# Kernel tuning notes

Hardware: AMD Instinct MI355X
Metric: run time of the kernel (lower is better)

Reference implementation:

```python
import jax, jax.numpy as jnp
import numpy as np

VOCAB = 512
EMB = 256
HID = 64
T_HORIZON = 0.05


def setup_inputs() -> dict:
    key = jax.random.key(0)
    ks = jax.random.split(key, 6)
    B, L = 32, 4096
    x = jax.random.randint(ks[0], (B, L), 0, VOCAB, dtype=jnp.int64 if jax.config.jax_enable_x64 else jnp.int32)
    emb_table = jax.random.normal(ks[1], (VOCAB, EMB), dtype=jnp.float32)
    W1 = jax.random.normal(ks[2], (EMB, HID), dtype=jnp.float32) * (1.0 / np.sqrt(EMB))
    b1 = jnp.zeros((HID,), dtype=jnp.float32)
    W2 = jax.random.normal(ks[3], (HID, VOCAB), dtype=jnp.float32) * (1.0 / np.sqrt(HID))
    b2 = jnp.full((VOCAB,), 0.1, dtype=jnp.float32)  # torch: bias.data.fill_(0.1)
    return {"x": x, "emb_table": emb_table, "W1": W1, "b1": b1, "W2": W2, "b2": b2, "steps": 5}


def reference(x, emb_table, W1, b1, W2, b2, steps):
    """Vectorized Gillespie-style Markov jump simulation.

    Equivalent to the torch loop: intensity is computed once per step from the
    current state, then every (b, l) position samples a candidate next state
    from softmax(intensity) with the self-transition zeroed and renormalized
    (== categorical over logits with the current state masked to -inf), and
    accepts it with prob 1 - exp(-rate * dt).
    """
    V = emb_table.shape[0]
    dt = T_HORIZON / steps
    key = jax.random.key(42)
    keys = jax.random.split(key, steps)
    vocab_ids = jnp.arange(V)

    def step(x_t, k):
        # intensity: [B, L, V]
        h = jax.nn.relu(emb_table[x_t] @ W1 + b1)
        intensity = h @ W2 + b2
        # mask self-transition (softmax * (1 - onehot) then renormalize)
        self_mask = x_t[..., None] == vocab_ids  # [B, L, V] bool
        masked_logits = jnp.where(self_mask, -jnp.inf, intensity)
        k1, k2 = jax.random.split(k)
        next_state = jax.random.categorical(k1, masked_logits)  # [B, L]
        rate = jnp.take_along_axis(intensity, next_state[..., None], axis=-1)[..., 0]
        accept_prob = 1.0 - jnp.exp(-rate * dt)
        u = jax.random.uniform(k2, x_t.shape, dtype=rate.dtype)
        x_t = jnp.where(u < accept_prob, next_state.astype(x_t.dtype), x_t)
        return x_t, None

    x_final, _ = jax.lax.scan(step, x, keys)
    return x_final
```

## Files before the change

### kernel.cpp

```cpp
#include <hip/hip_runtime.h>
#include <stdint.h>


#define VOCAB  512
#define EMB    256
#define HID    64
#define NPOS   (32 * 4096)
#define STEPS  5
#define PPW    8
#define CHUNKS (NPOS / PPW)
#define MBLK   2048
#define CPB    (CHUNKS / MBLK)

__host__ __device__ __forceinline__ void tf2x32(uint32_t k0, uint32_t k1,
                                                uint32_t x0, uint32_t x1,
                                                uint32_t& o0, uint32_t& o1) {
  uint32_t ks2 = k0 ^ k1 ^ 0x1BD11BDAu;
  x0 += k0; x1 += k1;
#define TFR(r) { x0 += x1; x1 = (x1 << (r)) | (x1 >> (32 - (r))); x1 ^= x0; }
  TFR(13) TFR(15) TFR(26) TFR(6)
  x0 += k1;  x1 += ks2 + 1u;
  TFR(17) TFR(29) TFR(16) TFR(24)
  x0 += ks2; x1 += k0 + 2u;
  TFR(13) TFR(15) TFR(26) TFR(6)
  x0 += k0;  x1 += k1 + 3u;
  TFR(17) TFR(29) TFR(16) TFR(24)
  x0 += k1;  x1 += ks2 + 4u;
  TFR(13) TFR(15) TFR(26) TFR(6)
  x0 += ks2; x1 += k0 + 5u;
#undef TFR
  o0 = x0; o1 = x1;
}

struct Keys {
  uint32_t k1a[STEPS], k1b[STEPS];
  uint32_t k2a[STEPS], k2b[STEPS];
};

__global__ __launch_bounds__(512)
void build_table(const float* __restrict__ emb,
                 const float* __restrict__ W1,
                 const float* __restrict__ b1,
                 const float* __restrict__ W2,
                 const float* __restrict__ b2,
                 float* __restrict__ I,
                 float* __restrict__ pthr) {
  const int s   = blockIdx.x;
  const int tid = threadIdx.x;
  __shared__ double part[8][HID];
  __shared__ double hd[HID];
  __shared__ float  redmax[8];

  const int hid = tid & (HID - 1);
  const int kq  = tid >> 6;
  const float* e = emb + s * EMB;
  double acc = 0.0;
#pragma unroll
  for (int ib = 0; ib < 32; ib += 16) {
    float ev[16], wv[16];
#pragma unroll
    for (int i = 0; i < 16; ++i) {
      const int k = kq + 8 * (ib + i);
      ev[i] = e[k];
      wv[i] = W1[k * HID + hid];
    }
#pragma unroll
    for (int i = 0; i < 16; ++i)
      acc += (double)ev[i] * (double)wv[i];
  }
  part[kq][hid] = acc;
  __syncthreads();
  if (kq == 0) {
    const double a = ((part[0][hid] + part[1][hid]) + (part[2][hid] + part[3][hid]))
                   + ((part[4][hid] + part[5][hid]) + (part[6][hid] + part[7][hid]));
    const float m = (float)a + b1[hid];
    hd[hid] = (double)(m > 0.0f ? m : 0.0f);
  }
  __syncthreads();

  double acc2 = 0.0;
#pragma unroll
  for (int kb = 0; kb < HID; kb += 16) {
    float wv[16];
#pragma unroll
    for (int i = 0; i < 16; ++i)
      wv[i] = W2[(kb + i) * VOCAB + tid];
#pragma unroll
    for (int i = 0; i < 16; ++i)
      acc2 += hd[kb + i] * (double)wv[i];
  }
  const float val = (float)acc2 + b2[tid];
  I[s * VOCAB + tid] = val;

  float lmax = val;
  for (int off = 32; off > 0; off >>= 1)
    lmax = fmaxf(lmax, __shfl_xor(lmax, off, 64));
  if ((tid & 63) == 0) redmax[tid >> 6] = lmax;
  __syncthreads();
  if (tid == 0) {
    float m = redmax[0];
#pragma unroll
    for (int i = 1; i < 8; ++i) m = fmaxf(m, redmax[i]);
    const float z = (-m) * 0.01f;
    pthr[s] = 1.0f - (float)exp((double)z);
  }
}

__global__ __launch_bounds__(256)
void markov_kernel(const int* __restrict__ x_in,
                   const float* __restrict__ I,
                   const float* __restrict__ pthr,
                   int* __restrict__ x_out,
                   Keys K) {
  __shared__ int next_chunk;
  if (threadIdx.x == 0) next_chunk = 0;
  __syncthreads();

  const int lane = threadIdx.x & 63;
  const int qp = lane / 5;
  const int qt = lane - qp * 5;
  const float TINYF = 1.17549435e-38f;

  for (;;) {
    int c = 0;
    if (lane == 0) c = atomicAdd(&next_chunk, 1);
    c = __shfl(c, 0, 64);
    if (c >= CPB) break;
    const int base = (blockIdx.x * CPB + c) * PPW;

    int scur = (lane < PPW) ? x_in[base + lane] : 0;
    const float pv = (lane < PPW) ? pthr[scur] : 0.0f;

    float u40 = 0.0f;
    if (lane < PPW * STEPS) {
      uint32_t w0, w1;
      tf2x32(K.k2a[qt], K.k2b[qt], 0u, (uint32_t)(base + qp), w0, w1);
      u40 = __uint_as_float((((w0 ^ w1) >> 9) | 0x3f800000u)) - 1.0f;
    }

    const float pq = __shfl(pv, qp, 64);
    const bool cand = (lane < PPW * STEPS) && (u40 < pq);
    unsigned long long mask = __ballot(cand);

    while (mask) {
      const int q = (int)__builtin_ctzll(mask);
      mask &= mask - 1;
      const int p = q / 5;
      const int t = q - p * 5;
      const int s = __builtin_amdgcn_readfirstlane(__shfl(scur, p, 64));

      const float* row = I + s * VOCAB;
      float rv[8];
#pragma unroll
      for (int j = 0; j < 8; ++j)
        rv[j] = row[lane + (j << 6)];

      const uint32_t fbase = ((uint32_t)(base + p) << 9) + (uint32_t)lane;
      uint32_t bits[8];
#pragma unroll
      for (int j = 0; j < 8; ++j) {
        uint32_t w0, w1;
        tf2x32(K.k1a[t], K.k1b[t], 0u, fbase + ((uint32_t)j << 6), w0, w1);
        bits[j] = w0 ^ w1;
      }

      float best = -__builtin_inff();
      float rbest = 0.0f;
      int bidx = 0;
#pragma unroll
      for (int j = 0; j < 8; ++j) {
        float ufv = __uint_as_float((bits[j] >> 9) | 0x3f800000u) - 1.0f;
        if (ufv == 0.0f) ufv = TINYF;
        const float g = -logf(-logf(ufv));
        const int v = lane + (j << 6);
        if (v != s) {
          const float val = rv[j] + g;
          if (val > best) { best = val; bidx = v; rbest = rv[j]; }
        }
      }
      for (int off = 32; off > 0; off >>= 1) {
        const float ob = __shfl_xor(best, off, 64);
        const int   oi = __shfl_xor(bidx, off, 64);
        const float orv = __shfl_xor(rbest, off, 64);
        if (ob > best || (ob == best && oi < bidx)) {
          best = ob; bidx = oi; rbest = orv;
        }
      }
      bidx = __builtin_amdgcn_readfirstlane(bidx);
      const float rate = rbest;
      const float z = (-rate) * 0.01f;
      const float pacc = 1.0f - (float)exp((double)z);
      const float u = __shfl(u40, q, 64);
      if (u < pacc) {
        if (lane == p) scur = bidx;
        const unsigned long long fut =
            (((1ull << (p * 5 + 5)) - 1) & ~((1ull << (q + 1)) - 1));
        const float pnew = pthr[bidx];
        const unsigned long long nb = __ballot(u40 < pnew) & fut;
        mask = (mask & ~fut) | nb;
      }
    }
    if (lane < PPW) x_out[base + lane] = scur;
  }
}

extern "C" void kernel_launch(void* const* d_in, const int* in_sizes, int n_in,
                              void* d_out, int out_size, void* d_ws, size_t ws_size,
                              hipStream_t stream) {
  const int*   x   = (const int*)d_in[0];
  const float* emb = (const float*)d_in[1];
  const float* W1  = (const float*)d_in[2];
  const float* b1  = (const float*)d_in[3];
  const float* W2  = (const float*)d_in[4];
  const float* b2  = (const float*)d_in[5];
  float* I    = (float*)d_ws;
  float* pthr = (float*)d_ws + VOCAB * VOCAB;
  int* out = (int*)d_out;

  Keys K;
  for (int t = 0; t < STEPS; ++t) {
    uint32_t Sa, Sb;
    tf2x32(0u, 42u, 0u, (uint32_t)t, Sa, Sb);
    tf2x32(Sa, Sb, 0u, 0u, K.k1a[t], K.k1b[t]);
    tf2x32(Sa, Sb, 0u, 1u, K.k2a[t], K.k2b[t]);
  }

  build_table<<<VOCAB, 512, 0, stream>>>(emb, W1, b1, W2, b2, I, pthr);
  markov_kernel<<<MBLK, 256, 0, stream>>>(x, I, pthr, out, K);
}
```

Baseline: 109.4 us.

## Filter Gumbel candidates with fast log, precompute acceptance-probability table

Candidate selection now runs in two passes. A cheap pass uses fast __logf to compute approximate Gumbel-perturbed logits and a wave-wide maximum. An exact precise-log pass then runs only on entries within a small margin of that maximum. The per-pair acceptance probability 1-exp(-0.01*I) is also precomputed into a second table in build_table, replacing the double-precision exp in the hot loop with one load. Exactness depends on the fast-log error staying below the margin, and the change adds a table write and extra workspace.

```diff
diff --git a/kernel.cpp b/kernel.cpp
--- a/kernel.cpp
+++ b/kernel.cpp
@@ -44,6 +44,7 @@
                  const float* __restrict__ W2,
                  const float* __restrict__ b2,
                  float* __restrict__ I,
+                 float* __restrict__ P,
                  float* __restrict__ pthr) {
   const int s   = blockIdx.x;
   const int tid = threadIdx.x;
@@ -91,8 +92,11 @@
   }
   const float val = (float)acc2 + b2[tid];
   I[s * VOCAB + tid] = val;
-
-  float lmax = val;
+  const float z = (-val) * 0.01f;
+  const float pv = 1.0f - (float)exp((double)z);
+  P[s * VOCAB + tid] = pv;
+
+  float lmax = pv;
   for (int off = 32; off > 0; off >>= 1)
     lmax = fmaxf(lmax, __shfl_xor(lmax, off, 64));
   if ((tid & 63) == 0) redmax[tid >> 6] = lmax;
@@ -101,14 +105,14 @@
     float m = redmax[0];
 #pragma unroll
     for (int i = 1; i < 8; ++i) m = fmaxf(m, redmax[i]);
-    const float z = (-m) * 0.01f;
-    pthr[s] = 1.0f - (float)exp((double)z);
+    pthr[s] = m;
   }
 }
 
 __global__ __launch_bounds__(256)
 void markov_kernel(const int* __restrict__ x_in,
                    const float* __restrict__ I,
+                   const float* __restrict__ P,
                    const float* __restrict__ pthr,
                    int* __restrict__ x_out,
                    Keys K) {
@@ -120,6 +124,7 @@
   const int qp = lane / 5;
   const int qt = lane - qp * 5;
   const float TINYF = 1.17549435e-38f;
+  const float NEGINF = -__builtin_inff();
 
   for (;;) {
     int c = 0;
@@ -164,32 +169,42 @@
         bits[j] = w0 ^ w1;
       }
 
-      float best = -__builtin_inff();
-      float rbest = 0.0f;
-      int bidx = 0;
+      float valC[8];
+      float bestC = NEGINF;
 #pragma unroll
       for (int j = 0; j < 8; ++j) {
         float ufv = __uint_as_float((bits[j] >> 9) | 0x3f800000u) - 1.0f;
         if (ufv == 0.0f) ufv = TINYF;
-        const float g = -logf(-logf(ufv));
+        const float gC = -__logf(-__logf(ufv));
         const int v = lane + (j << 6);
-        if (v != s) {
+        valC[j] = (v == s) ? NEGINF : rv[j] + gC;
+        bestC = fmaxf(bestC, valC[j]);
+      }
+      for (int off = 32; off > 0; off >>= 1)
+        bestC = fmaxf(bestC, __shfl_xor(bestC, off, 64));
+      const float thresh = bestC - 0.015625f;
+
+      float best = NEGINF;
+      int bidx = 0x7FFFFFFF;
+#pragma unroll
+      for (int j = 0; j < 8; ++j) {
+        if (valC[j] >= thresh) {
+          float ufv = __uint_as_float((bits[j] >> 9) | 0x3f800000u) - 1.0f;
+          if (ufv == 0.0f) ufv = TINYF;
+          const float g = -logf(-logf(ufv));
           const float val = rv[j] + g;
-          if (val > best) { best = val; bidx = v; rbest = rv[j]; }
+          const int v = lane + (j << 6);
+          if (val > best) { best = val; bidx = v; }
         }
       }
       for (int off = 32; off > 0; off >>= 1) {
         const float ob = __shfl_xor(best, off, 64);
         const int   oi = __shfl_xor(bidx, off, 64);
-        const float orv = __shfl_xor(rbest, off, 64);
-        if (ob > best || (ob == best && oi < bidx)) {
-          best = ob; bidx = oi; rbest = orv;
-        }
+        if (ob > best || (ob == best && oi < bidx)) { best = ob; bidx = oi; }
       }
       bidx = __builtin_amdgcn_readfirstlane(bidx);
-      const float rate = rbest;
-      const float z = (-rate) * 0.01f;
-      const float pacc = 1.0f - (float)exp((double)z);
+
+      const float pacc = P[s * VOCAB + bidx];
       const float u = __shfl(u40, q, 64);
       if (u < pacc) {
         if (lane == p) scur = bidx;
@@ -214,7 +229,8 @@
   const float* W2  = (const float*)d_in[4];
   const float* b2  = (const float*)d_in[5];
   float* I    = (float*)d_ws;
-  float* pthr = (float*)d_ws + VOCAB * VOCAB;
+  float* P    = I + VOCAB * VOCAB;
+  float* pthr = P + VOCAB * VOCAB;
   int* out = (int*)d_out;
 
   Keys K;
@@ -225,6 +241,6 @@
     tf2x32(Sa, Sb, 0u, 1u, K.k2a[t], K.k2b[t]);
   }
 
-  build_table<<<VOCAB, 512, 0, stream>>>(emb, W1, b1, W2, b2, I, pthr);
-  markov_kernel<<<MBLK, 256, 0, stream>>>(x, I, pthr, out, K);
-}
+  build_table<<<VOCAB, 512, 0, stream>>>(emb, W1, b1, W2, b2, I, P, pthr);
+  markov_kernel<<<MBLK, 256, 0, stream>>>(x, I, P, pthr, out, K);
+}
```

Measured after the change: 109.8 us. Within noise of the previous version (+0.4%).
